# Performance work log

Hardware: AMD Instinct MI355X
Metric: run time of the kernel (lower is better)

Reference implementation:

```python
import jax, jax.numpy as jnp
import numpy as np

LATENT = 100
INIT_SIZE = 8   # img_size // 4
NUM = 200       # LIF time steps
BETA = 0.95
THR = 1.0
CH_OUT = 3

# snntorch ATan surrogate spike (alpha=2 -> grad = 1/(1+(pi*u)^2))
@jax.custom_vjp
def spike_fn(x):
    return (x > 0).astype(x.dtype)

def _spike_fwd(x):
    return (x > 0).astype(x.dtype), x

def _spike_bwd(x, g):
    return (g / (1.0 + (jnp.pi * x) ** 2),)

spike_fn.defvjp(_spike_fwd, _spike_bwd)

def batchnorm(x, gamma, beta, eps):
    # training-mode BN: batch statistics over (N,H,W), biased variance (as torch)
    mean = x.mean(axis=(0, 2, 3), keepdims=True)
    var = ((x - mean) ** 2).mean(axis=(0, 2, 3), keepdims=True)
    xh = (x - mean) * jax.lax.rsqrt(var + eps)
    return xh * gamma[None, :, None, None] + beta[None, :, None, None]

def upsample2x(x):  # nearest-neighbor, scale 2
    return jnp.repeat(jnp.repeat(x, 2, axis=2), 2, axis=3)

def conv2d(x, w, b):  # 3x3, stride 1, padding 1
    y = jax.lax.conv_general_dilated(x, w, (1, 1), [(1, 1), (1, 1)],
                                     dimension_numbers=("NCHW", "OIHW", "NCHW"))
    return y + b[None, :, None, None]

def leaky_relu(x):
    return jnp.where(x >= 0, x, 0.2 * x)

def setup_inputs() -> dict:
    key = jax.random.key(0)
    ks = jax.random.split(key, 8)
    B = 8
    def n(k, shape, s=0.02):
        return jax.random.normal(k, shape, dtype=jnp.float32) * s
    return {
        "z": jax.random.normal(ks[0], (B, LATENT), dtype=jnp.float32),
        "w_l1": n(ks[1], (LATENT, 128 * INIT_SIZE ** 2)),
        "b_l1": jnp.zeros((128 * INIT_SIZE ** 2,), jnp.float32),
        "g1": jnp.ones((128,), jnp.float32), "be1": jnp.zeros((128,), jnp.float32),
        "w_c1": n(ks[2], (128, NUM * 128, 3, 3), 0.005),
        "b_c1": jnp.zeros((128,), jnp.float32),
        "g2": jnp.ones((128,), jnp.float32), "be2": jnp.zeros((128,), jnp.float32),
        "w_c2": n(ks[3], (64, 128, 3, 3)),
        "b_c2": jnp.zeros((64,), jnp.float32),
        "g3": jnp.ones((64,), jnp.float32), "be3": jnp.zeros((64,), jnp.float32),
        "w_c3": n(ks[4], (CH_OUT, 64, 3, 3)),
        "b_c3": jnp.zeros((CH_OUT,), jnp.float32),
    }

def reference(z, w_l1, b_l1, g1, be1, w_c1, b_c1, g2, be2, w_c2, b_c2, g3, be3, w_c3, b_c3):
    B = z.shape[0]
    out = z @ w_l1 + b_l1                       # (B, 128*8*8)
    out = out.reshape(B, 128, INIT_SIZE, INIT_SIZE)
    out = batchnorm(out, g1, be1, 1e-5)
    out = upsample2x(out)                       # (B,128,16,16) constant LIF input

    def lif_step(mem, _):
        # snntorch Leaky, reset-by-subtraction; reset detached from grad
        reset = jax.lax.stop_gradient((mem > THR).astype(mem.dtype))
        mem = BETA * mem + out - reset * THR
        spk = spike_fn(mem - THR)
        return mem, spk

    mem0 = jnp.zeros_like(out)
    _, spk_rec = jax.lax.scan(lif_step, mem0, None, length=NUM)  # (NUM,B,128,16,16)
    # faithful to torch.stack(dim=0).reshape(B, -1, 16, 16)
    x = spk_rec.reshape(B, NUM * 128, 16, 16)
    x = conv2d(x, w_c1, b_c1)                   # (B,128,16,16)
    x = leaky_relu(batchnorm(x, g2, be2, 0.8))  # BatchNorm2d(128, 0.8): eps=0.8
    x = upsample2x(x)                           # (B,128,32,32)
    x = conv2d(x, w_c2, b_c2)                   # (B,64,32,32)
    x = leaky_relu(batchnorm(x, g3, be3, 0.8))
    x = conv2d(x, w_c3, b_c3)                   # (B,3,32,32)
    return jnp.tanh(x)
```

## Files before the change

### kernel.cpp

```cpp
#include <hip/hip_runtime.h>
#include <math.h>


#define WROW 25632
#define SROW 25664

typedef _Float16 half8 __attribute__((ext_vector_type(8)));
typedef float f32x4 __attribute__((ext_vector_type(4)));
typedef unsigned int uint4v __attribute__((ext_vector_type(4)));

union AFrag { uint4v u4; unsigned int u[4]; half8 h; };

__global__ __launch_bounds__(256) void k_lin_bn1(
    const float* __restrict__ z, const float* __restrict__ w,
    const float* __restrict__ bias, const float* __restrict__ g1,
    const float* __restrict__ be1, float* __restrict__ I) {
  int ch = blockIdx.x, tid = threadIdx.x;
  __shared__ float red[256];
  int hw = tid & 63, b0 = tid >> 6;
  int j = ch * 64 + hw;
  float acc0 = bias[j], acc1 = acc0;
  const float* zp0 = z + b0 * 100;
  const float* zp1 = z + (b0 + 4) * 100;
  for (int l = 0; l < 100; ++l) {
    float wv = w[l * 8192 + j];
    acc0 += zp0[l] * wv;
    acc1 += zp1[l] * wv;
  }
  float v0 = acc0, v1 = acc1;
  red[tid] = v0 + v1; __syncthreads();
  for (int s = 128; s > 0; s >>= 1) { if (tid < s) red[tid] += red[tid + s]; __syncthreads(); }
  float mean = red[0] * (1.0f / 512.0f);
  __syncthreads();
  float d0 = v0 - mean, d1 = v1 - mean;
  red[tid] = d0 * d0 + d1 * d1; __syncthreads();
  for (int s = 128; s > 0; s >>= 1) { if (tid < s) red[tid] += red[tid + s]; __syncthreads(); }
  float var = red[0] * (1.0f / 512.0f);
  float coef = g1[ch] / sqrtf(var + 1e-5f);
  float beta = be1[ch];
  float q0 = (v0 - mean) * coef + beta;
  float q1 = (v1 - mean) * coef + beta;
#pragma unroll
  for (int k = 0; k < 2; ++k) {
    int n = k ? (tid + 256) : tid; float q = k ? q1 : q0;
    int b = n >> 6, hh = n & 63, h = hh >> 3, ww = hh & 7;
    float* o = I + (size_t)(b * 128 + ch) * 256 + (2 * h) * 16 + 2 * ww;
    o[0] = q; o[1] = q; o[16] = q; o[17] = q;
  }
}

__global__ __launch_bounds__(256) void k_lif(
    const float* __restrict__ I, unsigned char* __restrict__ spkTb) {
  int g = blockIdx.x * 256 + threadIdx.x;
  int px = g >> 10, plane = g & 1023;
  int lane = threadIdx.x & 63;
  float in = I[plane * 256 + px];
  int pos = ((px >> 4) + 1) * 18 + (px & 15) + 1;
  unsigned long long* wsrow =
      (unsigned long long*)(spkTb + (size_t)pos * SROW + ((plane - lane) >> 3));
  float mem = 0.0f;
  for (int t = 0; t < 200; ++t) {
    float reset = (mem > 1.0f) ? 1.0f : 0.0f;
    mem = 0.95f * mem + in - reset;
    unsigned long long m = __ballot(mem > 1.0f);
    if (lane == 0) wsrow[t * 16] = m;
  }
}

__global__ __launch_bounds__(256) void k_wtrans(
    const float* __restrict__ wc1, _Float16* __restrict__ wT) {
  __shared__ float t[2304];
  int oc = blockIdx.x / 100, cg = blockIdx.x % 100;
  int c0 = cg * 256, tid = threadIdx.x;
  const float* src = wc1 + (size_t)oc * 230400 + (size_t)c0 * 9;
#pragma unroll
  for (int i = 0; i < 9; ++i) t[tid + i * 256] = src[tid + i * 256];
  __syncthreads();
#pragma unroll
  for (int tap = 0; tap < 9; ++tap)
    wT[(size_t)(tap * 128 + oc) * WROW + c0 + tid] = (_Float16)t[tid * 9 + tap];
}

__device__ inline void expandp(unsigned int b, AFrag& f) {
  unsigned int lo = ((b & 0xFu) * 0x00204081u) & 0x01010101u;
  unsigned int hi = ((b >> 4) * 0x00204081u) & 0x01010101u;
  lo *= 0x3Cu; hi *= 0x3Cu;
  f.u[0] = __builtin_amdgcn_perm(0u, lo, 0x01040004u);
  f.u[1] = __builtin_amdgcn_perm(0u, lo, 0x03040204u);
  f.u[2] = __builtin_amdgcn_perm(0u, hi, 0x01040004u);
  f.u[3] = __builtin_amdgcn_perm(0u, hi, 0x03040204u);
}

__device__ __forceinline__ void gll16(const void* g, void* l) {
  __builtin_amdgcn_global_load_lds(
      (const __attribute__((address_space(1))) unsigned int*)g,
      (__attribute__((address_space(3))) unsigned int*)l, 16, 0, 0);
}

__global__ __launch_bounds__(256, 3) void k_conv1_mfma(
    const unsigned char* __restrict__ spkTb, const _Float16* __restrict__ wT,
    _Float16* __restrict__ y1p) {
  int v = (blockIdx.x & 7) * 96 + (blockIdx.x >> 3);
  int sl = v >> 4;
  int r = v & 15;
  int half = r >> 3, b = r & 7;
  int tid = threadIdx.x;
  int wave = tid >> 6, lane = tid & 63;
  int quad = lane >> 4, l16 = lane & 15;
  int qs = quad * 8;
  int h0 = wave * 4;

  int q0 = (sl * 25) / 6;
  int qc = ((sl + 1) * 25) / 6 - q0;
  int NBS = 9 * qc;

  __shared__ _Float16 As[2][8192];

  int ocl = tid >> 4;
  int sc0 = (tid & 15) ^ ocl;
  const char* srcA0 = (const char*)wT + (size_t)q0 * 256
                    + (size_t)(half * 64 + ocl) * (WROW * 2) + sc0 * 16;

  const unsigned char* rowp[4];
#pragma unroll
  for (int nt = 0; nt < 4; ++nt)
    rowp[nt] = spkTb + b * 3200 + q0 * 16
             + (size_t)((h0 + nt) * 18 + l16) * SROW;

  int dsb[4];
#pragma unroll
  for (int s = 0; s < 4; ++s)
    dsb[s] = l16 * 256 + ((s * 64 + quad * 16) ^ (l16 << 4));

  f32x4 acc[4][4] = {};

#pragma unroll
  for (int i = 0; i < 4; ++i)
    gll16(srcA0 + (size_t)i * (16 * WROW * 2), (char*)As + i * 4096 + wave * 1024);
  __syncthreads();

  int tap = 0, qi = 0;
  for (int k = 0; k < NBS; ++k) {
    int dh = tap / 3, dw = tap - dh * 3;
    uint4v bx[4];
    int boff = (dh * 18 + dw) * SROW + qi * 16;
#pragma unroll
    for (int nt = 0; nt < 4; ++nt)
      bx[nt] = *(const uint4v*)(rowp[nt] + boff);
    int qin = qi + 1, tapn = tap;
    if (qin == qc) { qin = 0; tapn = tap + 1; }
    if (k + 1 < NBS) {
      size_t aoff = (size_t)tapn * ((size_t)128 * WROW * 2) + (size_t)qin * 256;
      char* dst = (char*)As + ((k + 1) & 1) * 16384 + wave * 1024;
#pragma unroll
      for (int i = 0; i < 4; ++i)
        gll16(srcA0 + (size_t)i * (16 * WROW * 2) + aoff, dst + i * 4096);
    }
    const char* cA = (const char*)As + (k & 1) * 16384;
#pragma unroll
    for (int s = 0; s < 4; ++s) {
      AFrag a[4];
#pragma unroll
      for (int mt = 0; mt < 4; ++mt)
        a[mt].u4 = *(const uint4v*)(cA + dsb[s] + mt * 4096);
#pragma unroll
      for (int nt = 0; nt < 4; ++nt) {
        AFrag bf; expandp((bx[nt][s] >> qs) & 0xFFu, bf);
#pragma unroll
        for (int mt = 0; mt < 4; ++mt)
          acc[mt][nt] = __builtin_amdgcn_mfma_f32_16x16x32_f16(
              a[mt].h, bf.h, acc[mt][nt], 0, 0, 0);
      }
    }
    __syncthreads();
    tap = tapn; qi = qin;
  }

  _Float16* ob = y1p + (size_t)(sl * 8 + b) * 32768 + half * 16384;
#pragma unroll
  for (int mt = 0; mt < 4; ++mt)
#pragma unroll
    for (int nt = 0; nt < 4; ++nt) {
      int px = (h0 + nt) * 16 + l16;
#pragma unroll
      for (int rr = 0; rr < 4; ++rr) {
        int oc = mt * 16 + quad * 4 + rr;
        ob[(size_t)oc * 256 + px] = (_Float16)acc[mt][nt][rr];
      }
    }
}

__global__ __launch_bounds__(256) void k_bn2_up(
    const _Float16* __restrict__ y1p, const float* __restrict__ bc1,
    const float* __restrict__ g2, const float* __restrict__ be2,
    float* __restrict__ x2p) {
  int ch = blockIdx.x, tid = threadIdx.x;
  __shared__ float red[256];

  for (int e = tid; e < 1056; e += 256) {
    int b = e / 132, i = e - b * 132;
    int rr, cc;
    if (i < 34)       { rr = 0;       cc = i; }
    else if (i < 68)  { rr = 33;      cc = i - 34; }
    else if (i < 100) { rr = i - 67;  cc = 0; }
    else              { rr = i - 99;  cc = 33; }
    x2p[(size_t)(b * 128 + ch) * 1156 + rr * 34 + cc] = 0.0f;
  }

  int pp = tid & 127;
  int bh = tid >> 7;
  float bias = bc1[ch];
  float a[4][2] = {};
  const char* base = (const char*)y1p + ((size_t)ch * 256 + pp * 2) * 2
                   + (size_t)bh * 4 * 65536;
  for (int tl = 0; tl < 48; ++tl) {
    const char* q = base + (size_t)tl * 524288;
#pragma unroll
    for (int k = 0; k < 4; ++k) {
      union { unsigned int u; _Float16 h[2]; } cv;
      cv.u = *(const unsigned int*)(q + (size_t)k * 65536);
      a[k][0] += (float)cv.h[0];
      a[k][1] += (float)cv.h[1];
    }
  }
  float vv[4][2]; float s = 0.0f;
#pragma unroll
  for (int k = 0; k < 4; ++k)
#pragma unroll
    for (int e = 0; e < 2; ++e) { vv[k][e] = a[k][e] + bias; s += vv[k][e]; }

  red[tid] = s; __syncthreads();
  for (int st = 128; st > 0; st >>= 1) { if (tid < st) red[tid] += red[tid + st]; __syncthreads(); }
  float mean = red[0] * (1.0f / 2048.0f);
  __syncthreads();
  s = 0.0f;
#pragma unroll
  for (int k = 0; k < 4; ++k)
#pragma unroll
    for (int e = 0; e < 2; ++e) { float d = vv[k][e] - mean; s += d * d; }
  red[tid] = s; __syncthreads();
  for (int st = 128; st > 0; st >>= 1) { if (tid < st) red[tid] += red[tid + st]; __syncthreads(); }
  float var = red[0] * (1.0f / 2048.0f);
  float coef = g2[ch] / sqrtf(var + 0.8f);
  float beta = be2[ch];
#pragma unroll
  for (int k = 0; k < 4; ++k)
#pragma unroll
    for (int e = 0; e < 2; ++e) {
      int b = bh * 4 + k, px = pp * 2 + e, h = px >> 4, w = px & 15;
      float q = (vv[k][e] - mean) * coef + beta;
      q = (q >= 0.0f) ? q : 0.2f * q;
      float* o = x2p + (size_t)(b * 128 + ch) * 1156 + (2 * h + 1) * 34 + (2 * w + 1);
      o[0] = q; o[1] = q; o[34] = q; o[35] = q;
    }
}

__global__ __launch_bounds__(256) void k_conv2(
    const float* __restrict__ x2p, const float* __restrict__ wc2,
    const float* __restrict__ bc2, float* __restrict__ y2) {
  int octile = blockIdx.x, b = blockIdx.y, pq = blockIdx.z;
  int tid = threadIdx.x;
  int p = pq * 256 + tid, h = p >> 5, w = p & 31;
  float a0 = 0.0f, a1 = 0.0f, a2 = 0.0f, a3 = 0.0f;
  const float* base = x2p + (size_t)(b * 128) * 1156 + h * 34 + w;
  const float* wb = wc2 + (size_t)(octile * 4) * 128 * 9;
  for (int ch = 0; ch < 128; ++ch) {
    const float* pp = base + (size_t)ch * 1156;
    float s0 = pp[0],  s1 = pp[1],  s2 = pp[2];
    float s3 = pp[34], s4 = pp[35], s5 = pp[36];
    float s6 = pp[68], s7 = pp[69], s8 = pp[70];
    const float* w0 = wb + (size_t)ch * 9;
    const float* w1 = wb + (size_t)(128 + ch) * 9;
    const float* w2 = wb + (size_t)(256 + ch) * 9;
    const float* w3 = wb + (size_t)(384 + ch) * 9;
    a0 += s0*w0[0]+s1*w0[1]+s2*w0[2]+s3*w0[3]+s4*w0[4]+s5*w0[5]+s6*w0[6]+s7*w0[7]+s8*w0[8];
    a1 += s0*w1[0]+s1*w1[1]+s2*w1[2]+s3*w1[3]+s4*w1[4]+s5*w1[5]+s6*w1[6]+s7*w1[7]+s8*w1[8];
    a2 += s0*w2[0]+s1*w2[1]+s2*w2[2]+s3*w2[3]+s4*w2[4]+s5*w2[5]+s6*w2[6]+s7*w2[7]+s8*w2[8];
    a3 += s0*w3[0]+s1*w3[1]+s2*w3[2]+s3*w3[3]+s4*w3[4]+s5*w3[5]+s6*w3[6]+s7*w3[7]+s8*w3[8];
  }
  int oc0 = octile * 4;
  y2[(size_t)(b * 64 + oc0 + 0) * 1024 + p] = a0 + bc2[oc0 + 0];
  y2[(size_t)(b * 64 + oc0 + 1) * 1024 + p] = a1 + bc2[oc0 + 1];
  y2[(size_t)(b * 64 + oc0 + 2) * 1024 + p] = a2 + bc2[oc0 + 2];
  y2[(size_t)(b * 64 + oc0 + 3) * 1024 + p] = a3 + bc2[oc0 + 3];
}

__global__ __launch_bounds__(256) void k_bn3(
    const float* __restrict__ y2, const float* __restrict__ g3,
    const float* __restrict__ be3, float* __restrict__ y2n) {
  int ch = blockIdx.x, tid = threadIdx.x;
  __shared__ float red[256];

  for (int e = tid; e < 1056; e += 256) {
    int b = e / 132, i = e - b * 132;
    int rr, cc;
    if (i < 34)       { rr = 0;       cc = i; }
    else if (i < 68)  { rr = 33;      cc = i - 34; }
    else if (i < 100) { rr = i - 67;  cc = 0; }
    else              { rr = i - 99;  cc = 33; }
    y2n[(size_t)(b * 64 + ch) * 1156 + rr * 34 + cc] = 0.0f;
  }

  float v[32]; float s = 0.0f;
#pragma unroll
  for (int k = 0; k < 32; ++k) {
    int n = tid + k * 256;
    v[k] = y2[(size_t)((n >> 10) * 64 + ch) * 1024 + (n & 1023)];
    s += v[k];
  }
  red[tid] = s; __syncthreads();
  for (int st = 128; st > 0; st >>= 1) { if (tid < st) red[tid] += red[tid + st]; __syncthreads(); }
  float mean = red[0] * (1.0f / 8192.0f);
  __syncthreads();
  s = 0.0f;
#pragma unroll
  for (int k = 0; k < 32; ++k) { float d = v[k] - mean; s += d * d; }
  red[tid] = s; __syncthreads();
  for (int st = 128; st > 0; st >>= 1) { if (tid < st) red[tid] += red[tid + st]; __syncthreads(); }
  float var = red[0] * (1.0f / 8192.0f);
  float coef = g3[ch] / sqrtf(var + 0.8f);
  float beta = be3[ch];
#pragma unroll
  for (int k = 0; k < 32; ++k) {
    int n = tid + k * 256;
    int b = n >> 10, px = n & 1023, h = px >> 5, w = px & 31;
    float q = (v[k] - mean) * coef + beta;
    q = (q >= 0.0f) ? q : 0.2f * q;
    y2n[(size_t)(b * 64 + ch) * 1156 + (h + 1) * 34 + (w + 1)] = q;
  }
}

__global__ __launch_bounds__(256) void k_conv3(
    const float* __restrict__ y2n, const float* __restrict__ wc3,
    const float* __restrict__ bc3, float* __restrict__ out) {
  int b = blockIdx.x >> 4, pg = blockIdx.x & 15;
  int tid = threadIdx.x;
  int pxl = tid & 63, cg = tid >> 6;
  int p = pg * 64 + pxl, h = p >> 5, w = p & 31;
  float a0 = 0.0f, a1 = 0.0f, a2 = 0.0f;
  const float* base = y2n + (size_t)(b * 64 + cg * 16) * 1156 + h * 34 + w;
  for (int c = 0; c < 16; ++c) {
    int ch = cg * 16 + c;
    const float* pp = base + (size_t)c * 1156;
    float s0 = pp[0],  s1 = pp[1],  s2 = pp[2];
    float s3 = pp[34], s4 = pp[35], s5 = pp[36];
    float s6 = pp[68], s7 = pp[69], s8 = pp[70];
    const float* w0 = wc3 + (size_t)ch * 9;
    const float* w1 = wc3 + (size_t)(64 + ch) * 9;
    const float* w2 = wc3 + (size_t)(128 + ch) * 9;
    a0 += s0*w0[0]+s1*w0[1]+s2*w0[2]+s3*w0[3]+s4*w0[4]+s5*w0[5]+s6*w0[6]+s7*w0[7]+s8*w0[8];
    a1 += s0*w1[0]+s1*w1[1]+s2*w1[2]+s3*w1[3]+s4*w1[4]+s5*w1[5]+s6*w1[6]+s7*w1[7]+s8*w1[8];
    a2 += s0*w2[0]+s1*w2[1]+s2*w2[2]+s3*w2[3]+s4*w2[4]+s5*w2[5]+s6*w2[6]+s7*w2[7]+s8*w2[8];
  }
  __shared__ float red[3][256];
  red[0][tid] = a0; red[1][tid] = a1; red[2][tid] = a2;
  __syncthreads();
  if (tid < 192) {
    int oc = tid >> 6, px = tid & 63;
    float sres = red[oc][px] + red[oc][px + 64] + red[oc][px + 128] + red[oc][px + 192];
    out[(size_t)(b * 3 + oc) * 1024 + pg * 64 + px] = tanhf(sres + bc3[oc]);
  }
}

extern "C" void kernel_launch(void* const* d_in, const int* in_sizes, int n_in,
                              void* d_out, int out_size, void* d_ws, size_t ws_size,
                              hipStream_t stream) {
  const float* z    = (const float*)d_in[0];
  const float* w_l1 = (const float*)d_in[1];
  const float* b_l1 = (const float*)d_in[2];
  const float* g1   = (const float*)d_in[3];
  const float* be1  = (const float*)d_in[4];
  const float* w_c1 = (const float*)d_in[5];
  const float* b_c1 = (const float*)d_in[6];
  const float* g2   = (const float*)d_in[7];
  const float* be2  = (const float*)d_in[8];
  const float* w_c2 = (const float*)d_in[9];
  const float* b_c2 = (const float*)d_in[10];
  const float* g3   = (const float*)d_in[11];
  const float* be3  = (const float*)d_in[12];
  const float* w_c3 = (const float*)d_in[13];
  const float* b_c3 = (const float*)d_in[14];
  float* out = (float*)d_out;

  char* ws = (char*)d_ws;
  _Float16* wT = (_Float16*)ws;
  unsigned char* spkTb = (unsigned char*)(ws + 59056128);
  float* I   = (float*)(ws + 67633408);
  _Float16* y1p = (_Float16*)(ws + 69730560);
  float* x2p = (float*)ws;
  float* y2n = (float*)(ws + 4734976);
  float* y2  = (float*)(ws + 7102464);

  size_t spkTb_bytes = (size_t)324 * SROW;

  hipMemsetAsync(spkTb, 0, spkTb_bytes, stream);

  k_wtrans <<<12800, 256, 0, stream>>>(w_c1, wT);
  k_lin_bn1<<<128, 256, 0, stream>>>(z, w_l1, b_l1, g1, be1, I);
  k_lif    <<<1024, 256, 0, stream>>>(I, spkTb);
  k_conv1_mfma<<<768, 256, 0, stream>>>(spkTb, wT, y1p);

  k_bn2_up <<<128, 256, 0, stream>>>(y1p, b_c1, g2, be2, x2p);
  k_conv2  <<<dim3(16, 8, 4), 256, 0, stream>>>(x2p, w_c2, b_c2, y2);
  k_bn3    <<<64, 256, 0, stream>>>(y2, g3, be3, y2n);
  k_conv3  <<<128, 256, 0, stream>>>(y2n, w_c3, b_c3, out);
}
```

Baseline: 437.0 us.

## Zero spike halo in LIF kernel, pack weight transpose, prefetch conv1 B operands

Drops the full memset of the spike buffer and instead has the LIF kernel zero only the padding halo rows (top, bottom, left/right border columns). The weight transpose kernel now handles two output channels per block and writes packed pairs of halves as 32-bit stores, halving the block count. The conv1 MFMA loop prefetches the next iteration's spike B-operand into registers alongside the A async load and replaces per-iteration tap division with incremental offsets. These cut memset traffic, narrow-store overhead, and B-load latency, at the cost of more registers in conv1.

```diff
diff --git a/kernel.cpp b/kernel.cpp
--- a/kernel.cpp
+++ b/kernel.cpp
@@ -52,6 +52,15 @@
 __global__ __launch_bounds__(256) void k_lif(
     const float* __restrict__ I, unsigned char* __restrict__ spkTb) {
   int g = blockIdx.x * 256 + threadIdx.x;
+  if (g < 217600) {
+    int hr = g / 3200;
+    int i  = g - hr * 3200;
+    int row;
+    if (hr < 18)      row = hr;
+    else if (hr < 36) row = 306 + (hr - 18);
+    else { int kk = hr - 36; row = ((kk >> 1) + 1) * 18 + ((kk & 1) ? 17 : 0); }
+    *(unsigned long long*)(spkTb + (size_t)row * SROW + (size_t)i * 8) = 0ULL;
+  }
   int px = g >> 10, plane = g & 1023;
   int lane = threadIdx.x & 63;
   float in = I[plane * 256 + px];
@@ -69,16 +78,26 @@
 
 __global__ __launch_bounds__(256) void k_wtrans(
     const float* __restrict__ wc1, _Float16* __restrict__ wT) {
-  __shared__ float t[2304];
-  int oc = blockIdx.x / 100, cg = blockIdx.x % 100;
-  int c0 = cg * 256, tid = threadIdx.x;
-  const float* src = wc1 + (size_t)oc * 230400 + (size_t)c0 * 9;
-#pragma unroll
-  for (int i = 0; i < 9; ++i) t[tid + i * 256] = src[tid + i * 256];
-  __syncthreads();
-#pragma unroll
-  for (int tap = 0; tap < 9; ++tap)
-    wT[(size_t)(tap * 128 + oc) * WROW + c0 + tid] = (_Float16)t[tid * 9 + tap];
+  __shared__ float t[2][2304];
+  int op = blockIdx.x / 100, cg = blockIdx.x % 100;
+  int oc0 = op * 2, c0 = cg * 256, tid = threadIdx.x;
+  const float* src = wc1 + (size_t)oc0 * 230400 + (size_t)c0 * 9;
+#pragma unroll
+  for (int i = 0; i < 9; ++i) {
+    t[0][tid + i * 256] = src[tid + i * 256];
+    t[1][tid + i * 256] = src[230400 + tid + i * 256];
+  }
+  __syncthreads();
+  int oh = tid >> 7;
+  int cp = tid & 127;
+#pragma unroll
+  for (int tap = 0; tap < 9; ++tap) {
+    union { unsigned int u; _Float16 h[2]; } pk;
+    pk.h[0] = (_Float16)t[oh][(2 * cp) * 9 + tap];
+    pk.h[1] = (_Float16)t[oh][(2 * cp + 1) * 9 + tap];
+    *(unsigned int*)((char*)wT +
+        ((size_t)(tap * 128 + oc0 + oh) * WROW + c0 + 2 * cp) * 2) = pk.u;
+  }
 }
 
 __device__ inline void expandp(unsigned int b, AFrag& f) {
@@ -133,28 +152,38 @@
     dsb[s] = l16 * 256 + ((s * 64 + quad * 16) ^ (l16 << 4));
 
   f32x4 acc[4][4] = {};
+  uint4v bx[4], bxn[4];
 
 #pragma unroll
   for (int i = 0; i < 4; ++i)
     gll16(srcA0 + (size_t)i * (16 * WROW * 2), (char*)As + i * 4096 + wave * 1024);
-  __syncthreads();
-
-  int tap = 0, qi = 0;
+#pragma unroll
+  for (int nt = 0; nt < 4; ++nt)
+    bx[nt] = *(const uint4v*)(rowp[nt]);
+  __syncthreads();
+
+  size_t atap = 0;
+  int btap = 0, dw = 0;
+  int qi = 0;
   for (int k = 0; k < NBS; ++k) {
-    int dh = tap / 3, dw = tap - dh * 3;
-    uint4v bx[4];
-    int boff = (dh * 18 + dw) * SROW + qi * 16;
-#pragma unroll
-    for (int nt = 0; nt < 4; ++nt)
-      bx[nt] = *(const uint4v*)(rowp[nt] + boff);
-    int qin = qi + 1, tapn = tap;
-    if (qin == qc) { qin = 0; tapn = tap + 1; }
+    int qin = qi + 1;
+    size_t atapn = atap; int btapn = btap; int dwn = dw;
+    if (qin == qc) {
+      qin = 0;
+      atapn = atap + (size_t)128 * (WROW * 2);
+      btapn = btap + ((dw == 2) ? 16 * SROW : SROW);
+      dwn = (dw == 2) ? 0 : dw + 1;
+    }
     if (k + 1 < NBS) {
-      size_t aoff = (size_t)tapn * ((size_t)128 * WROW * 2) + (size_t)qin * 256;
+      int bo = btapn + qin * 16;
+#pragma unroll
+      for (int nt = 0; nt < 4; ++nt)
+        bxn[nt] = *(const uint4v*)(rowp[nt] + bo);
+      const char* sA = srcA0 + atapn + (size_t)(qin * 256);
       char* dst = (char*)As + ((k + 1) & 1) * 16384 + wave * 1024;
 #pragma unroll
       for (int i = 0; i < 4; ++i)
-        gll16(srcA0 + (size_t)i * (16 * WROW * 2) + aoff, dst + i * 4096);
+        gll16(sA + (size_t)i * (16 * WROW * 2), dst + i * 4096);
     }
     const char* cA = (const char*)As + (k & 1) * 16384;
 #pragma unroll
@@ -173,7 +202,11 @@
       }
     }
     __syncthreads();
-    tap = tapn; qi = qin;
+    if (k + 1 < NBS) {
+#pragma unroll
+      for (int nt = 0; nt < 4; ++nt) bx[nt] = bxn[nt];
+    }
+    qi = qin; atap = atapn; btap = btapn; dw = dwn;
   }
 
   _Float16* ob = y1p + (size_t)(sl * 8 + b) * 32768 + half * 16384;
@@ -391,11 +424,7 @@
   float* y2n = (float*)(ws + 4734976);
   float* y2  = (float*)(ws + 7102464);
 
-  size_t spkTb_bytes = (size_t)324 * SROW;
-
-  hipMemsetAsync(spkTb, 0, spkTb_bytes, stream);
-
-  k_wtrans <<<12800, 256, 0, stream>>>(w_c1, wT);
+  k_wtrans <<<6400, 256, 0, stream>>>(w_c1, wT);
   k_lin_bn1<<<128, 256, 0, stream>>>(z, w_l1, b_l1, g1, be1, I);
   k_lif    <<<1024, 256, 0, stream>>>(I, spkTb);
   k_conv1_mfma<<<768, 256, 0, stream>>>(spkTb, wT, y1p);
```

Result: no change. 436.1 us (-0.2%).
